# Kernel optimization log

Hardware: AMD Instinct MI355X
Metric: run time of the kernel (lower is better)

Reference implementation:

```python
import jax, jax.numpy as jnp
import numpy as np

B, S, D = 2, 2048, 2048
H, HKV = 16, 4
GROUPS = H // HKV
RQ, RKV = 1024, 512
DH, DR = 192, 64          # q_head_dim, rope dim
DN = DH - DR              # nrope dim = 128
DV = 128                  # v head dim
EPS = 1e-20


def setup_inputs() -> dict:
    key = jax.random.key(0)
    ks = jax.random.split(key, 8)
    inp = {
        "hidden_states": jax.random.normal(ks[0], (B, S, D), jnp.float32),
        # causal mask (0 = masked), as used by masked_fill(mask == 0, -inf)
        "attention_mask": jnp.tril(jnp.ones((S, S), jnp.int32))[None, None],
        "w_qa": jax.random.normal(ks[1], (D, RQ), jnp.float32) * 0.02,
        "b_qa": jnp.zeros((RQ,), jnp.float32),
        "g_q": jnp.ones((RQ,), jnp.float32),
        "w_qb": jax.random.normal(ks[2], (RQ, H * DH), jnp.float32) * 0.02,
        "b_qb": jnp.zeros((H * DH,), jnp.float32),
        "w_kva": jax.random.normal(ks[3], (D, RKV + DR), jnp.float32) * 0.02,
        "b_kva": jnp.zeros((RKV + DR,), jnp.float32),
        "g_kv": jnp.ones((RKV,), jnp.float32),
        "w_kvb": jax.random.normal(ks[4], (RKV, HKV * (DN + DV)), jnp.float32) * 0.02,
        "b_kvb": jnp.zeros((HKV * (DN + DV),), jnp.float32),
        "w_o": jax.random.normal(ks[5], (H * DV, D), jnp.float32) * 0.02,
        "b_o": jnp.zeros((D,), jnp.float32),
    }
    return inp


def _rmsnorm(x, g, eps=EPS):
    var = jnp.mean(x * x, axis=-1, keepdims=True)
    return x * jax.lax.rsqrt(var + eps) * g


def _rope_cos_sin(seq_len, dim, base=10000.0, dtype=jnp.float32):
    inv_freq = 1.0 / (base ** (jnp.arange(0, dim, 2, dtype=jnp.float32) / dim))
    t = jnp.arange(seq_len, dtype=jnp.float32)
    freqs = jnp.outer(t, inv_freq)                    # [S, dim/2]
    emb = jnp.concatenate([freqs, freqs], axis=-1)    # [S, dim]
    return jnp.cos(emb).astype(dtype), jnp.sin(emb).astype(dtype)


def _apply_rope(x, cos, sin):
    # x: [..., S, dr]; rotate_half convention
    d2 = x.shape[-1] // 2
    x1, x2 = x[..., :d2], x[..., d2:]
    rot = jnp.concatenate([-x2, x1], axis=-1)
    return x * cos + rot * sin


def reference(hidden_states, attention_mask, w_qa, b_qa, g_q, w_qb, b_qb,
              w_kva, b_kva, g_kv, w_kvb, b_kvb, w_o, b_o):
    b, s, _ = hidden_states.shape
    # --- Q: LoRA down -> RMSNorm -> LoRA up ---
    q_a = hidden_states @ w_qa + b_qa                         # [B,S,RQ]
    q_b = _rmsnorm(q_a, g_q) @ w_qb + b_qb                    # [B,S,H*DH]
    q_b = q_b.reshape(b, s, H, DH).transpose(0, 2, 1, 3)      # [B,H,S,DH]
    q_nrope, q_rope = q_b[..., :DN], q_b[..., DN:]
    # --- KV: LoRA down, split latent / shared rope key ---
    kv_a = hidden_states @ w_kva + b_kva                      # [B,S,RKV+DR]
    kv_c, k_rope = kv_a[..., :RKV], kv_a[..., RKV:]
    kv_b = _rmsnorm(kv_c, g_kv) @ w_kvb + b_kvb               # [B,S,HKV*(DN+DV)]
    kv_b = kv_b.reshape(b, s, HKV, DN + DV).transpose(0, 2, 1, 3)
    k_nrope, value_states = kv_b[..., :DN], kv_b[..., DN:]    # [B,HKV,S,DN/DV]
    # --- split RoPE ---
    cos, sin = _rope_cos_sin(s, DR, dtype=hidden_states.dtype)
    q_rope = _apply_rope(q_rope, cos, sin)                    # [B,H,S,DR]
    k_rope = _apply_rope(k_rope[:, None], cos, sin)           # [B,1,S,DR]
    # --- assemble heads (rope part first, matching source concat order) ---
    query_states = jnp.concatenate([q_rope, q_nrope], axis=-1)            # [B,H,S,DH]
    key_states = jnp.concatenate(
        [jnp.broadcast_to(k_rope, (b, HKV, s, DR)), k_nrope], axis=-1)    # [B,HKV,S,DH]
    # --- GQA expand kv heads ---
    key_states = jnp.repeat(key_states, GROUPS, axis=1)                   # [B,H,S,DH]
    value_states = jnp.repeat(value_states, GROUPS, axis=1)               # [B,H,S,DV]
    # --- attention ---
    scores = jnp.einsum('bhqd,bhkd->bhqk', query_states, key_states)
    scores = scores / jnp.sqrt(jnp.asarray(DH, scores.dtype))
    scores = jnp.where(attention_mask == 0, jnp.asarray(-1e9, scores.dtype), scores)
    weights = jax.nn.softmax(scores, axis=-1)
    attn_out = jnp.einsum('bhqk,bhkd->bhqd', weights, value_states)       # [B,H,S,DV]
    attn_out = attn_out.transpose(0, 2, 1, 3).reshape(b, s, H * DV)
    return attn_out @ w_o + b_o
```

## Files before the change

### kernel.cpp

```cpp
#include <hip/hip_runtime.h>
#include <hip/hip_bf16.h>
#include <stdint.h>

#define DEV static __device__ __forceinline__

typedef __attribute__((ext_vector_type(8))) short bf16x8;
typedef __attribute__((ext_vector_type(4))) float f32x4;
typedef __attribute__((ext_vector_type(16))) float f32x16;

constexpr int Bc = 2, Sc = 2048, Dc = 2048;
constexpr int Hc = 16, HKVc = 4;
constexpr int RQc = 1024, RKVc = 512;
constexpr int DHc = 192, DRc = 64, DVc = 128;

DEV unsigned short f2bf(float f) {
  union { float f; uint32_t u; } v; v.f = f;
  uint32_t r = v.u + 0x7FFFu + ((v.u >> 16) & 1u);
  return (unsigned short)(r >> 16);
}
DEV float bf2f(unsigned short u) {
  union { uint32_t u; float f; } v; v.u = ((uint32_t)u) << 16;
  return v.f;
}

DEV void gload_lds16(const unsigned short* g, unsigned short* l) {
  __builtin_amdgcn_global_load_lds(
      (const __attribute__((address_space(1))) unsigned int*)g,
      (__attribute__((address_space(3))) unsigned int*)l, 16, 0, 0);
}

__global__ void f2b_kernel(const float* __restrict__ in, unsigned short* __restrict__ out, int n) {
  int stride = gridDim.x * blockDim.x;
  for (int i = blockIdx.x * blockDim.x + threadIdx.x; i * 4 < n; i += stride) {
    float4 v = reinterpret_cast<const float4*>(in)[i];
    union { unsigned short u[4]; uint64_t q; } pk;
    pk.u[0] = f2bf(v.x); pk.u[1] = f2bf(v.y); pk.u[2] = f2bf(v.z); pk.u[3] = f2bf(v.w);
    reinterpret_cast<uint64_t*>(out)[i] = pk.q;
  }
}

__global__ void wtrans_kernel(const float* __restrict__ in, unsigned short* __restrict__ out,
                              int R, int C) {
  __shared__ float tile[32][33];
  const int c0 = blockIdx.x * 32, r0 = blockIdx.y * 32;
  const int tx = threadIdx.x & 31, ty = threadIdx.x >> 5;
#pragma unroll
  for (int i = 0; i < 32; i += 8)
    tile[ty + i][tx] = in[(size_t)(r0 + ty + i) * C + c0 + tx];
  __syncthreads();
#pragma unroll
  for (int i = 0; i < 32; i += 8)
    out[(size_t)(c0 + ty + i) * R + r0 + tx] = f2bf(tile[tx][ty + i]);
}

__global__ void rope_table_kernel(float* __restrict__ cosT, float* __restrict__ sinT) {
  int idx = blockIdx.x * blockDim.x + threadIdx.x;
  if (idx >= Sc * DRc) return;
  int t = idx >> 6;
  int j = idx & 63;
  float inv = exp2f(-13.287712379549449f * (float)(j & 31) * (1.0f / 32.0f));
  float f = (float)t * inv;
  cosT[idx] = cosf(f);
  sinT[idx] = sinf(f);
}

template<int R>
__global__ void rmsnorm_kernel(const float* __restrict__ in, int istride,
                               const float* __restrict__ g, unsigned short* __restrict__ out) {
  int row = blockIdx.x;
  const float* x = in + (size_t)row * istride;
  float ss = 0.f;
  for (int j = threadIdx.x; j < R; j += 256) { float v = x[j]; ss += v * v; }
  for (int off = 32; off; off >>= 1) ss += __shfl_down(ss, off, 64);
  __shared__ float wsum[4];
  if ((threadIdx.x & 63) == 0) wsum[threadIdx.x >> 6] = ss;
  __syncthreads();
  float tot = wsum[0] + wsum[1] + wsum[2] + wsum[3];
  float rs = rsqrtf(tot * (1.0f / R) + 1e-20f);
  for (int j = threadIdx.x; j < R; j += 256)
    out[(size_t)row * R + j] = f2bf(x[j] * rs * g[j]);
}

template<bool OUT_BF16, bool NG>
__global__ __launch_bounds__(256)
void gemm_tn_kernel(const unsigned short* __restrict__ A, const unsigned short* __restrict__ Bt,
                    const float* __restrict__ bias, void* __restrict__ Cout,
                    int M, int N, int K) {
  __shared__ __align__(16) unsigned short As[128 * 64];
  __shared__ __align__(16) unsigned short Bs[128 * 64];
  const int t = threadIdx.x, lane = t & 63, wave = t >> 6;
  const int wm = wave >> 1, wn = wave & 1;
  const int m0 = blockIdx.x * 128, n0 = blockIdx.y * 128;
  const int fr = lane & 15, fo = (lane >> 4) * 8, rg = lane >> 4;
  const int srow = lane >> 3;
  const int scol = (lane & 7) * 8;

  const unsigned short* Ap[4];
  const unsigned short* Bp[4];
#pragma unroll
  for (int i = 0; i < 4; ++i) {
    const int ar = m0 + wave * 32 + i * 8 + srow;
    Ap[i] = A + (size_t)ar * K + scol;
    int br = n0 + wave * 32 + i * 8 + srow;
    if (NG) br = br < N ? br : N - 1;
    Bp[i] = Bt + (size_t)br * K + scol;
  }

  f32x4 acc[4][4] = {};

  for (int k0 = 0; k0 < K; k0 += 64) {
    if (k0) __syncthreads();
#pragma unroll
    for (int i = 0; i < 4; ++i) {
      gload_lds16(Ap[i] + k0, &As[(wave * 32 + i * 8) * 64]);
      gload_lds16(Bp[i] + k0, &Bs[(wave * 32 + i * 8) * 64]);
    }
    asm volatile("s_waitcnt vmcnt(0)" ::: "memory");
    __syncthreads();
#pragma unroll
    for (int kk = 0; kk < 64; kk += 32) {
      bf16x8 af[4], bf[4];
#pragma unroll
      for (int m = 0; m < 4; ++m)
        af[m] = *reinterpret_cast<const bf16x8*>(&As[(wm * 64 + m * 16 + fr) * 64 + kk + fo]);
#pragma unroll
      for (int n = 0; n < 4; ++n)
        bf[n] = *reinterpret_cast<const bf16x8*>(&Bs[(wn * 64 + n * 16 + fr) * 64 + kk + fo]);
      __builtin_amdgcn_s_setprio(1);
#pragma unroll
      for (int m = 0; m < 4; ++m)
#pragma unroll
        for (int n = 0; n < 4; ++n)
          acc[m][n] = __builtin_amdgcn_mfma_f32_16x16x32_bf16(af[m], bf[n], acc[m][n], 0, 0, 0);
      __builtin_amdgcn_s_setprio(0);
    }
  }

#pragma unroll
  for (int m = 0; m < 4; ++m) {
    const int row = m0 + wm * 64 + m * 16 + rg * 4;
#pragma unroll
    for (int n = 0; n < 4; ++n) {
      const int col = n0 + wn * 64 + n * 16 + fr;
      if (NG && col >= N) continue;
      const float bb = bias[col];
#pragma unroll
      for (int r = 0; r < 4; ++r) {
        float v = acc[m][n][r] + bb;
        if (OUT_BF16)
          reinterpret_cast<unsigned short*>(Cout)[(size_t)(row + r) * N + col] = f2bf(v);
        else
          reinterpret_cast<float*>(Cout)[(size_t)(row + r) * N + col] = v;
      }
    }
  }
}

__global__ __launch_bounds__(256)
void gemm_qfuse_kernel(const unsigned short* __restrict__ A, const unsigned short* __restrict__ Bt,
                       const float* __restrict__ bias,
                       const float* __restrict__ cosT, const float* __restrict__ sinT,
                       unsigned short* __restrict__ Qt, int M, int N, int K) {
  const float QS = 0.07216878364870323f * 1.4426950408889634f;
  __shared__ __align__(16) unsigned short As[128 * 64];
  __shared__ __align__(16) unsigned short Bs[128 * 64];
  const int t = threadIdx.x, lane = t & 63, wave = t >> 6;
  const int wm = wave >> 1, wn = wave & 1;
  const int m0 = blockIdx.x * 128, n0 = blockIdx.y * 128;
  const int fr = lane & 15, fo = (lane >> 4) * 8, rg = lane >> 4;
  const int srow = lane >> 3;
  const int scol = (lane & 7) * 8;

  const unsigned short* Ap[4];
  const unsigned short* Bp[4];
#pragma unroll
  for (int i = 0; i < 4; ++i) {
    Ap[i] = A + (size_t)(m0 + wave * 32 + i * 8 + srow) * K + scol;
    Bp[i] = Bt + (size_t)(n0 + wave * 32 + i * 8 + srow) * K + scol;
  }

  f32x4 acc[4][4] = {};

  for (int k0 = 0; k0 < K; k0 += 64) {
    if (k0) __syncthreads();
#pragma unroll
    for (int i = 0; i < 4; ++i) {
      gload_lds16(Ap[i] + k0, &As[(wave * 32 + i * 8) * 64]);
      gload_lds16(Bp[i] + k0, &Bs[(wave * 32 + i * 8) * 64]);
    }
    asm volatile("s_waitcnt vmcnt(0)" ::: "memory");
    __syncthreads();
#pragma unroll
    for (int kk = 0; kk < 64; kk += 32) {
      bf16x8 af[4], bf[4];
#pragma unroll
      for (int m = 0; m < 4; ++m)
        af[m] = *reinterpret_cast<const bf16x8*>(&As[(wm * 64 + m * 16 + fr) * 64 + kk + fo]);
#pragma unroll
      for (int n = 0; n < 4; ++n)
        bf[n] = *reinterpret_cast<const bf16x8*>(&Bs[(wn * 64 + n * 16 + fr) * 64 + kk + fo]);
      __builtin_amdgcn_s_setprio(1);
#pragma unroll
      for (int m = 0; m < 4; ++m)
#pragma unroll
        for (int n = 0; n < 4; ++n)
          acc[m][n] = __builtin_amdgcn_mfma_f32_16x16x32_bf16(af[m], bf[n], acc[m][n], 0, 0, 0);
      __builtin_amdgcn_s_setprio(0);
    }
  }

  const int wbase = n0 + wn * 64;
  const int hq = wbase / 192;
  const int dbase = wbase - hq * 192;
  const bool ropewin = (dbase == 128);

#pragma unroll
  for (int m = 0; m < 4; ++m) {
    const int row0 = m0 + wm * 64 + m * 16 + rg * 4;
#pragma unroll
    for (int n = 0; n < 4; ++n) {
      const int col = wbase + n * 16 + fr;
      const int d = dbase + n * 16 + fr;
      const float bb = bias[col];
#pragma unroll
      for (int r = 0; r < 4; ++r) {
        const int row = row0 + r;
        const int s = row & (Sc - 1);
        const int bq = row >> 11;
        float qv = acc[m][n][r] + bb;
        if (ropewin) {
          const int j = d - 128;
          const int n2 = (n < 2) ? n + 2 : n - 2;
          const float pv = acc[m][n2][r] + bias[wbase + n2 * 16 + fr];
          const float c = cosT[s * 64 + j], sn = sinT[s * 64 + j];
          qv = (n < 2) ? (qv * c - pv * sn) : (qv * c + pv * sn);
        }
        Qt[((size_t)(bq * Hc + hq) * Sc + s) * DHc + d] = f2bf(qv * QS);
      }
    }
  }
}

__global__ void prep_k_kernel(const unsigned short* __restrict__ kvb,
                              const float* __restrict__ ccat,
                              const float* __restrict__ cosT, const float* __restrict__ sinT,
                              unsigned short* __restrict__ K) {
  int bs = blockIdx.x;
  int s = bs & (Sc - 1);
  int b = bs >> 11;
  int d = threadIdx.x;
  if (d >= 192) return;
  unsigned short ropeval = 0;
  if (d >= 128) {
    int j = d - 128;
    float x = ccat[(size_t)bs * 1600 + 1536 + j];
    float other = ccat[(size_t)bs * 1600 + 1536 + (j < 32 ? j + 32 : j - 32)];
    float c = cosT[s * 64 + j], sn = sinT[s * 64 + j];
    float v = (j < 32) ? (x * c - other * sn) : (x * c + other * sn);
    ropeval = f2bf(v);
  }
  const size_t off = (size_t)(s >> 5) * 6144 + (d >> 3) * 256 + (s & 31) * 8 + (d & 7);
  for (int kvh = 0; kvh < HKVc; ++kvh) {
    unsigned short o;
    if (d < 128) o = kvb[(size_t)bs * 1024 + kvh * 256 + d];
    else o = ropeval;
    K[(size_t)(b * HKVc + kvh) * Sc * DHc + off] = o;
  }
}

__global__ void vtrans_kernel(const unsigned short* __restrict__ kvb, unsigned short* __restrict__ Vt) {
  int idx = blockIdx.x;
  int dt = idx & 3;  idx >>= 2;
  int st = idx & 63; idx >>= 6;
  int kvh = idx & 3; idx >>= 2;
  int b = idx;
  __shared__ unsigned short tile[32][33];
  int t = threadIdx.x;
  int c = t & 31, r0 = t >> 5;
#pragma unroll
  for (int i = 0; i < 4; ++i) {
    int r = r0 + i * 8;
    int s = st * 32 + r;
    tile[r][c] = kvb[((size_t)(b * Sc + s)) * 1024 + kvh * 256 + 128 + dt * 32 + c];
  }
  __syncthreads();
#pragma unroll
  for (int i = 0; i < 4; ++i) {
    int r = r0 + i * 8;
    const int dd = dt * 32 + r;
    const int k = st * 32 + c;
    const size_t pos = (size_t)(k >> 5) * 4096 + ((k >> 3) & 3) * 1024 + dd * 8 + (k & 7);
    Vt[(size_t)((b * HKVc + kvh)) * DVc * Sc + pos] = tile[c][r];
  }
}

__global__ __launch_bounds__(128, 3)
void attn_kernel(const unsigned short* __restrict__ Q, const unsigned short* __restrict__ Kt,
                 const unsigned short* __restrict__ Vt, unsigned short* __restrict__ attnOut) {
  __shared__ __align__(16) unsigned short Ks[2][6144];

  const int bid = blockIdx.x;
  const int g = bid & 7;
  const int b = g >> 2, kvh = g & 3;
  const int idx = bid >> 3;
  const int hp = idx & 1;
  const int sub = 63 - (idx >> 1);
  const int w = threadIdx.x >> 6;
  const int h = kvh * 4 + hp * 2 + w;
  const int lane = threadIdx.x & 63;
  const int l31 = lane & 31, hi = lane >> 5;

  const unsigned short* Qh = Q + (size_t)(b * Hc + h) * Sc * DHc;
  const unsigned short* Kg = Kt + (size_t)(b * HKVc + kvh) * Sc * DHc;
  const unsigned short* Vg = Vt + (size_t)(b * HKVc + kvh) * DVc * Sc;

  const int q0 = sub * 32;
  const int q = q0 + l31;
  const int NT = sub + 1;

  auto stage = [&](int t) {
    const unsigned short* src = Kg + (size_t)t * 6144;
    unsigned short* dst = &Ks[t & 1][0];
#pragma unroll
    for (int j = 0; j < 6; ++j) {
      const int jj = w * 6 + j;
      gload_lds16(src + jj * 512 + lane * 8, dst + jj * 512);
    }
  };

  bf16x8 qf[12];
#pragma unroll
  for (int f = 0; f < 12; ++f)
    qf[f] = *reinterpret_cast<const bf16x8*>(Qh + (size_t)q * DHc + f * 16 + hi * 8);

  f32x16 ot[4] = {};
  float m = -INFINITY, lsum = 0.f;

  stage(0);
  asm volatile("s_waitcnt vmcnt(0)" ::: "memory");
  __syncthreads();

  for (int t = 0; t < NT; ++t) {
    const int cur = t & 1;

    bf16x8 vf[8];
#pragma unroll
    for (int dt = 0; dt < 4; ++dt)
#pragma unroll
      for (int k2 = 0; k2 < 2; ++k2)
        vf[dt * 2 + k2] = *reinterpret_cast<const bf16x8*>(
            Vg + (size_t)t * 4096 + (k2 * 2 + hi) * 1024 + (dt * 32 + l31) * 8);
    __builtin_amdgcn_sched_barrier(0);
    if (t + 1 < NT) stage(t + 1);
    __builtin_amdgcn_sched_barrier(0);

    const unsigned short* kb = &Ks[cur][0];
    f32x16 s = {};
    __builtin_amdgcn_s_setprio(1);
#pragma unroll
    for (int f = 0; f < 12; ++f) {
      bf16x8 kf = *reinterpret_cast<const bf16x8*>(kb + (f * 2 + hi) * 256 + l31 * 8);
      s = __builtin_amdgcn_mfma_f32_32x32x16_bf16(kf, qf[f], s, 0, 0, 0);
    }
    __builtin_amdgcn_s_setprio(0);

    float v[16];
    if (t == sub) {
#pragma unroll
      for (int rrr = 0; rrr < 16; ++rrr) {
        const int kl = (rrr & 3) + 8 * (rrr >> 2) + 4 * hi;
        v[rrr] = (kl <= l31) ? s[rrr] : -3.0e38f;
      }
    } else {
#pragma unroll
      for (int rrr = 0; rrr < 16; ++rrr) v[rrr] = s[rrr];
    }

    float pmax = fmaxf(fmaxf(fmaxf(v[0], v[1]), fmaxf(v[2], v[3])),
                       fmaxf(fmaxf(v[4], v[5]), fmaxf(v[6], v[7])));
    float pmax2 = fmaxf(fmaxf(fmaxf(v[8], v[9]), fmaxf(v[10], v[11])),
                        fmaxf(fmaxf(v[12], v[13]), fmaxf(v[14], v[15])));
    pmax = fmaxf(pmax, pmax2);
    pmax = fmaxf(pmax, __shfl_xor(pmax, 32, 64));

    float cf = 1.f;
    if (!__all(pmax - m <= 8.0f)) {
      const float mnew = fmaxf(m, pmax);
      cf = exp2f(m - mnew);
      m = mnew;
#pragma unroll
      for (int dt = 0; dt < 4; ++dt)
#pragma unroll
        for (int rrr = 0; rrr < 16; ++rrr) ot[dt][rrr] *= cf;
    }

    float pp[16];
    float rs = 0.f;
#pragma unroll
    for (int rrr = 0; rrr < 16; ++rrr) { pp[rrr] = exp2f(v[rrr] - m); rs += pp[rrr]; }
    rs += __shfl_xor(rs, 32, 64);
    lsum = lsum * cf + rs;

    uint32_t c[8], x[8];
#pragma unroll
    for (int ii = 0; ii < 8; ++ii) {
      asm("v_cvt_pk_bf16_f32 %0, %1, %2" : "=v"(c[ii]) : "v"(pp[2 * ii]), "v"(pp[2 * ii + 1]));
      x[ii] = (uint32_t)__shfl_xor((int)c[ii], 32, 64);
    }
    union { uint32_t w[4]; bf16x8 v8; } pa0, pa1;
    pa0.w[0] = hi ? x[2] : c[0];
    pa0.w[1] = hi ? x[3] : c[1];
    pa0.w[2] = hi ? c[2] : x[0];
    pa0.w[3] = hi ? c[3] : x[1];
    pa1.w[0] = hi ? x[6] : c[4];
    pa1.w[1] = hi ? x[7] : c[5];
    pa1.w[2] = hi ? c[6] : x[4];
    pa1.w[3] = hi ? c[7] : x[5];

    __builtin_amdgcn_s_setprio(1);
#pragma unroll
    for (int dt = 0; dt < 4; ++dt) {
      ot[dt] = __builtin_amdgcn_mfma_f32_32x32x16_bf16(vf[dt * 2], pa0.v8, ot[dt], 0, 0, 0);
      ot[dt] = __builtin_amdgcn_mfma_f32_32x32x16_bf16(vf[dt * 2 + 1], pa1.v8, ot[dt], 0, 0, 0);
    }
    __builtin_amdgcn_s_setprio(0);

    asm volatile("s_waitcnt vmcnt(0)" ::: "memory");
    __syncthreads();
  }

  const float inv = 1.0f / lsum;
  unsigned short* dst = attnOut + ((size_t)(b * Sc + q)) * (Hc * DVc) + h * DVc;
#pragma unroll
  for (int dt = 0; dt < 4; ++dt)
#pragma unroll
    for (int rq = 0; rq < 4; ++rq) {
      uint32_t lo = (uint32_t)f2bf(ot[dt][rq * 4 + 0] * inv) |
                    ((uint32_t)f2bf(ot[dt][rq * 4 + 1] * inv) << 16);
      uint32_t hi2 = (uint32_t)f2bf(ot[dt][rq * 4 + 2] * inv) |
                     ((uint32_t)f2bf(ot[dt][rq * 4 + 3] * inv) << 16);
      uint2 pk; pk.x = lo; pk.y = hi2;
      *reinterpret_cast<uint2*>(dst + dt * 32 + 8 * rq + 4 * hi) = pk;
    }
}

extern "C" void kernel_launch(void* const* d_in, const int* in_sizes, int n_in,
                              void* d_out, int out_size, void* d_ws, size_t ws_size,
                              hipStream_t stream) {
  (void)in_sizes; (void)n_in; (void)out_size; (void)ws_size;
  const float* hidden = (const float*)d_in[0];
  const float* w_qa  = (const float*)d_in[2];
  const float* b_qa  = (const float*)d_in[3];
  const float* g_q   = (const float*)d_in[4];
  const float* w_qb  = (const float*)d_in[5];
  const float* b_qb  = (const float*)d_in[6];
  const float* w_kva = (const float*)d_in[7];
  const float* b_kva = (const float*)d_in[8];
  const float* g_kv  = (const float*)d_in[9];
  const float* w_kvb = (const float*)d_in[10];
  const float* b_kvb = (const float*)d_in[11];
  const float* w_o   = (const float*)d_in[12];
  const float* b_o   = (const float*)d_in[13];
  float* out = (float*)d_out;

  char* ws = (char*)d_ws;
  size_t off = 0;
  auto alloc = [&](size_t bytes) -> void* {
    void* p = ws + off;
    off += (bytes + 255) & ~(size_t)255;
    return p;
  };
  const int MS = Bc * Sc;
  const int NCAT = RQc + RKVc + DRc;

  unsigned short* Xbf   = (unsigned short*)alloc((size_t)MS * Dc * 2);
  unsigned short* Wcat  = (unsigned short*)alloc((size_t)NCAT * Dc * 2);
  unsigned short* WqbT  = (unsigned short*)alloc((size_t)Hc * DHc * RQc * 2);
  unsigned short* WkvbT = (unsigned short*)alloc((size_t)HKVc * 256 * RKVc * 2);
  unsigned short* WoT   = (unsigned short*)alloc((size_t)Dc * Hc * DVc * 2);
  float* bcat = (float*)alloc((size_t)NCAT * 4);
  float* cosT = (float*)alloc((size_t)Sc * DRc * 4);
  float* sinT = (float*)alloc((size_t)Sc * DRc * 4);
  float* Ccat = (float*)alloc((size_t)MS * NCAT * 4);
  unsigned short* qan  = (unsigned short*)alloc((size_t)MS * RQc * 2);
  unsigned short* kvcn = (unsigned short*)alloc((size_t)MS * RKVc * 2);
  unsigned short* kvb  = (unsigned short*)alloc((size_t)MS * HKVc * 256 * 2);
  unsigned short* Qt   = (unsigned short*)alloc((size_t)Bc * Hc * Sc * DHc * 2);
  unsigned short* Kt   = (unsigned short*)alloc((size_t)Bc * HKVc * Sc * DHc * 2);
  unsigned short* Vt   = (unsigned short*)alloc((size_t)Bc * HKVc * DVc * Sc * 2);
  unsigned short* attnb= (unsigned short*)alloc((size_t)MS * Hc * DVc * 2);

  f2b_kernel<<<dim3(512), dim3(256), 0, stream>>>(hidden, Xbf, MS * Dc);
  wtrans_kernel<<<dim3(RQc / 32, Dc / 32), 256, 0, stream>>>(w_qa, Wcat, Dc, RQc);
  wtrans_kernel<<<dim3((RKVc + DRc) / 32, Dc / 32), 256, 0, stream>>>(w_kva, Wcat + (size_t)RQc * Dc, Dc, RKVc + DRc);
  wtrans_kernel<<<dim3(Hc * DHc / 32, RQc / 32), 256, 0, stream>>>(w_qb, WqbT, RQc, Hc * DHc);
  wtrans_kernel<<<dim3(HKVc * 256 / 32, RKVc / 32), 256, 0, stream>>>(w_kvb, WkvbT, RKVc, HKVc * 256);
  wtrans_kernel<<<dim3(Dc / 32, Hc * DVc / 32), 256, 0, stream>>>(w_o, WoT, Hc * DVc, Dc);
  hipMemcpyAsync(bcat, b_qa, (size_t)RQc * 4, hipMemcpyDeviceToDevice, stream);
  hipMemcpyAsync(bcat + RQc, b_kva, (size_t)(RKVc + DRc) * 4, hipMemcpyDeviceToDevice, stream);
  rope_table_kernel<<<dim3(512), dim3(256), 0, stream>>>(cosT, sinT);

  gemm_tn_kernel<false, true><<<dim3(MS / 128, (NCAT + 127) / 128), 256, 0, stream>>>(Xbf, Wcat, bcat, Ccat, MS, NCAT, Dc);
  rmsnorm_kernel<1024><<<dim3(MS), 256, 0, stream>>>(Ccat, NCAT, g_q, qan);
  rmsnorm_kernel<512><<<dim3(MS), 256, 0, stream>>>(Ccat + RQc, NCAT, g_kv, kvcn);
  gemm_qfuse_kernel<<<dim3(MS / 128, Hc * DHc / 128), 256, 0, stream>>>(qan, WqbT, b_qb, cosT, sinT, Qt, MS, Hc * DHc, RQc);
  gemm_tn_kernel<true, false><<<dim3(MS / 128, HKVc * 256 / 128), 256, 0, stream>>>(kvcn, WkvbT, b_kvb, kvb, MS, HKVc * 256, RKVc);

  prep_k_kernel<<<dim3(MS), 256, 0, stream>>>(kvb, Ccat, cosT, sinT, Kt);
  vtrans_kernel<<<dim3(Bc * HKVc * (Sc / 32) * (DVc / 32)), 256, 0, stream>>>(kvb, Vt);

  attn_kernel<<<dim3(1024), dim3(128), 0, stream>>>(Qt, Kt, Vt, attnb);

  gemm_tn_kernel<false, false><<<dim3(MS / 128, Dc / 128), 256, 0, stream>>>(attnb, WoT, b_o, out, MS, Dc, Hc * DVc);
}
```

Baseline: 322.3 us.

## Split long causal attention rows across two KV halves and merge partial results

The 32 longest query tiles (rows 1024 to 2047) are now each split into two blocks that cover different halves of the KV range. Each half writes its unnormalised fp32 output plus its running max and sum to scratch. A new merge kernel rescales and combines the two halves and writes the bf16 attention output. The goal is to balance work across the causal triangle and reduce the tail, at the cost of an extra launch, more fp32 scratch traffic, and reusing the Ccat buffer as scratch. That scratch extends past Ccat into the adjacent allocation.

```diff
diff --git a/kernel.cpp b/kernel.cpp
--- a/kernel.cpp
+++ b/kernel.cpp
@@ -296,15 +296,20 @@
 
 __global__ __launch_bounds__(128, 3)
 void attn_kernel(const unsigned short* __restrict__ Q, const unsigned short* __restrict__ Kt,
-                 const unsigned short* __restrict__ Vt, unsigned short* __restrict__ attnOut) {
+                 const unsigned short* __restrict__ Vt, unsigned short* __restrict__ attnOut,
+                 float* __restrict__ Opart, float* __restrict__ mlp) {
   __shared__ __align__(16) unsigned short Ks[2][6144];
 
   const int bid = blockIdx.x;
   const int g = bid & 7;
   const int b = g >> 2, kvh = g & 3;
-  const int idx = bid >> 3;
-  const int hp = idx & 1;
-  const int sub = 63 - (idx >> 1);
+  const int u = bid >> 3;
+  int sub, hp, half; bool split;
+  if (u < 128) {
+    split = true; sub = 63 - (u >> 2); half = (u >> 1) & 1; hp = u & 1;
+  } else {
+    split = false; const int v = u - 128; sub = 31 - (v >> 1); hp = v & 1; half = 0;
+  }
   const int w = threadIdx.x >> 6;
   const int h = kvh * 4 + hp * 2 + w;
   const int lane = threadIdx.x & 63;
@@ -317,6 +322,9 @@
   const int q0 = sub * 32;
   const int q = q0 + l31;
   const int NT = sub + 1;
+  const int tmid = (sub + 2) >> 1;
+  const int t0 = (split && half) ? tmid : 0;
+  const int t1 = split ? (half ? NT : tmid) : NT;
 
   auto stage = [&](int t) {
     const unsigned short* src = Kg + (size_t)t * 6144;
@@ -336,11 +344,11 @@
   f32x16 ot[4] = {};
   float m = -INFINITY, lsum = 0.f;
 
-  stage(0);
+  stage(t0);
   asm volatile("s_waitcnt vmcnt(0)" ::: "memory");
   __syncthreads();
 
-  for (int t = 0; t < NT; ++t) {
+  for (int t = t0; t < t1; ++t) {
     const int cur = t & 1;
 
     bf16x8 vf[8];
@@ -351,7 +359,7 @@
         vf[dt * 2 + k2] = *reinterpret_cast<const bf16x8*>(
             Vg + (size_t)t * 4096 + (k2 * 2 + hi) * 1024 + (dt * 32 + l31) * 8);
     __builtin_amdgcn_sched_barrier(0);
-    if (t + 1 < NT) stage(t + 1);
+    if (t + 1 < t1) stage(t + 1);
     __builtin_amdgcn_sched_barrier(0);
 
     const unsigned short* kb = &Ks[cur][0];
@@ -429,19 +437,73 @@
     __syncthreads();
   }
 
-  const float inv = 1.0f / lsum;
-  unsigned short* dst = attnOut + ((size_t)(b * Sc + q)) * (Hc * DVc) + h * DVc;
-#pragma unroll
-  for (int dt = 0; dt < 4; ++dt)
-#pragma unroll
-    for (int rq = 0; rq < 4; ++rq) {
-      uint32_t lo = (uint32_t)f2bf(ot[dt][rq * 4 + 0] * inv) |
-                    ((uint32_t)f2bf(ot[dt][rq * 4 + 1] * inv) << 16);
-      uint32_t hi2 = (uint32_t)f2bf(ot[dt][rq * 4 + 2] * inv) |
-                     ((uint32_t)f2bf(ot[dt][rq * 4 + 3] * inv) << 16);
-      uint2 pk; pk.x = lo; pk.y = hi2;
-      *reinterpret_cast<uint2*>(dst + dt * 32 + 8 * rq + 4 * hi) = pk;
-    }
+  if (!split) {
+    const float inv = 1.0f / lsum;
+    unsigned short* dst = attnOut + ((size_t)(b * Sc + q)) * (Hc * DVc) + h * DVc;
+#pragma unroll
+    for (int dt = 0; dt < 4; ++dt)
+#pragma unroll
+      for (int rq = 0; rq < 4; ++rq) {
+        uint32_t lo = (uint32_t)f2bf(ot[dt][rq * 4 + 0] * inv) |
+                      ((uint32_t)f2bf(ot[dt][rq * 4 + 1] * inv) << 16);
+        uint32_t hi2 = (uint32_t)f2bf(ot[dt][rq * 4 + 2] * inv) |
+                       ((uint32_t)f2bf(ot[dt][rq * 4 + 3] * inv) << 16);
+        uint2 pk; pk.x = lo; pk.y = hi2;
+        *reinterpret_cast<uint2*>(dst + dt * 32 + 8 * rq + 4 * hi) = pk;
+      }
+  } else {
+    const int bh = b * Hc + h;
+    const int rowid = (bh << 10) + (q - 1024);
+    float* Op = Opart + ((size_t)(half * 32768 + rowid)) * 128;
+#pragma unroll
+    for (int dt = 0; dt < 4; ++dt)
+#pragma unroll
+      for (int rq = 0; rq < 4; ++rq) {
+        float4 vv;
+        vv.x = ot[dt][rq * 4 + 0];
+        vv.y = ot[dt][rq * 4 + 1];
+        vv.z = ot[dt][rq * 4 + 2];
+        vv.w = ot[dt][rq * 4 + 3];
+        *reinterpret_cast<float4*>(Op + dt * 32 + 8 * rq + 4 * hi) = vv;
+      }
+    if (hi == 0) {
+      mlp[((size_t)half * 32768 + rowid) * 2] = m;
+      mlp[((size_t)half * 32768 + rowid) * 2 + 1] = lsum;
+    }
+  }
+}
+
+__global__ __launch_bounds__(256)
+void attn_merge_kernel(const float* __restrict__ Opart, const float* __restrict__ mlp,
+                       unsigned short* __restrict__ attnOut) {
+  const int rowid = blockIdx.x * 16 + (threadIdx.x >> 4);
+  const int dd = (threadIdx.x & 15) * 8;
+  const int bh = rowid >> 10, qm = rowid & 1023;
+  const int b = bh >> 4, h = bh & 15;
+  const int q = 1024 + qm;
+  const float m0 = mlp[(size_t)rowid * 2];
+  const float l0 = mlp[(size_t)rowid * 2 + 1];
+  const float m1 = mlp[((size_t)32768 + rowid) * 2];
+  const float l1 = mlp[((size_t)32768 + rowid) * 2 + 1];
+  const float ms = fmaxf(m0, m1);
+  const float s0 = exp2f(m0 - ms), s1 = exp2f(m1 - ms);
+  const float inv = 1.0f / (l0 * s0 + l1 * s1);
+  const float* P0 = Opart + (size_t)rowid * 128 + dd;
+  const float* P1 = Opart + ((size_t)32768 + rowid) * 128 + dd;
+  float4 a0 = reinterpret_cast<const float4*>(P0)[0];
+  float4 a1 = reinterpret_cast<const float4*>(P0)[1];
+  float4 b0 = reinterpret_cast<const float4*>(P1)[0];
+  float4 b1 = reinterpret_cast<const float4*>(P1)[1];
+  union { unsigned short u[8]; uint4 v; } pk;
+  pk.u[0] = f2bf((a0.x * s0 + b0.x * s1) * inv);
+  pk.u[1] = f2bf((a0.y * s0 + b0.y * s1) * inv);
+  pk.u[2] = f2bf((a0.z * s0 + b0.z * s1) * inv);
+  pk.u[3] = f2bf((a0.w * s0 + b0.w * s1) * inv);
+  pk.u[4] = f2bf((a1.x * s0 + b1.x * s1) * inv);
+  pk.u[5] = f2bf((a1.y * s0 + b1.y * s1) * inv);
+  pk.u[6] = f2bf((a1.z * s0 + b1.z * s1) * inv);
+  pk.u[7] = f2bf((a1.w * s0 + b1.w * s1) * inv);
+  *reinterpret_cast<uint4*>(attnOut + ((size_t)(b * Sc + q)) * (Hc * DVc) + h * DVc + dd) = pk.v;
 }
 
 extern "C" void kernel_launch(void* const* d_in, const int* in_sizes, int n_in,
@@ -490,6 +552,9 @@
   unsigned short* Vt   = (unsigned short*)alloc((size_t)Bc * HKVc * DVc * Sc * 2);
   unsigned short* attnb= (unsigned short*)alloc((size_t)MS * Hc * DVc * 2);
 
+  float* Opart = Ccat;
+  float* mlp = Ccat + (size_t)2 * 32768 * 128;
+
   f2b_kernel<<<dim3(512), dim3(256), 0, stream>>>(hidden, Xbf, MS * Dc);
   wtrans_kernel<<<dim3(RQc / 32, Dc / 32), 256, 0, stream>>>(w_qa, Wcat, Dc, RQc);
   wtrans_kernel<<<dim3((RKVc + DRc) / 32, Dc / 32), 256, 0, stream>>>(w_kva, Wcat + (size_t)RQc * Dc, Dc, RKVc + DRc);
@@ -509,7 +574,8 @@
   prep_k_kernel<<<dim3(MS), 256, 0, stream>>>(kvb, Ccat, cosT, sinT, Kt);
   vtrans_kernel<<<dim3(Bc * HKVc * (Sc / 32) * (DVc / 32)), 256, 0, stream>>>(kvb, Vt);
 
-  attn_kernel<<<dim3(1024), dim3(128), 0, stream>>>(Qt, Kt, Vt, attnb);
+  attn_kernel<<<dim3(1536), dim3(128), 0, stream>>>(Qt, Kt, Vt, attnb, Opart, mlp);
+  attn_merge_kernel<<<dim3(2048), dim3(256), 0, stream>>>(Opart, mlp, attnb);
 
   gemm_tn_kernel<false, false><<<dim3(MS / 128, Dc / 128), 256, 0, stream>>>(attnb, WoT, b_o, out, MS, Dc, Hc * DVc);
 }
```

Result: no change. 325.8 us (+1.1%).
